# Optimization experiments

Hardware: AMD Instinct MI355X
Metric: run time of the kernel (lower is better)

The kernel has to match this reference:

```python
import jax, jax.numpy as jnp
import numpy as np

N, E, F_DIM = 30000, 480000, 256
CLS_HID, NUM_CLASS, GEN_HID, MI_HID, BATCH = 128, 16, 64, 128, 4096
COM_L1, COM_L2, LAM, ALPHA, TAU, EPS = 0.5, 0.5, 0.5, 1.0, 0.5, 1e-8


def _glorot(key, shape):
    scale = jnp.sqrt(2.0 / (shape[0] + shape[-1]))
    return scale * jax.random.normal(key, shape, dtype=jnp.float32)


def setup_inputs() -> dict:
    key = jax.random.key(0)
    ks = jax.random.split(key, 32)
    inp = {
        'feat': jax.random.normal(ks[0], (N, F_DIM), dtype=jnp.float32),
        'view1_indices': jax.random.randint(ks[1], (2, E), 0, N),
        'view1_values': jax.random.uniform(ks[2], (E,), dtype=jnp.float32),
        'view2_indices': jax.random.randint(ks[3], (2, E), 0, N),
        'view2_values': jax.random.uniform(ks[4], (E,), dtype=jnp.float32),
        'idx': jnp.sort(jax.random.randint(ks[5], (BATCH,), 0, N)),
        # GenView (v1 and v2): gen_gcn weight + gen_mlp (Linear(2*gen_hid, 1))
        'W_gen_v1': _glorot(ks[6], (F_DIM, GEN_HID)),
        'Wm_v1': _glorot(ks[7], (2 * GEN_HID, 1)),
        'bm_v1': jnp.zeros((1,), dtype=jnp.float32),
        'W_gen_v2': _glorot(ks[8], (F_DIM, GEN_HID)),
        'Wm_v2': _glorot(ks[9], (2 * GEN_HID, 1)),
        'bm_v2': jnp.zeros((1,), dtype=jnp.float32),
        # Classification: three two-layer GCN encoders (v1, v2, v)
        'W1_v1': _glorot(ks[10], (F_DIM, CLS_HID)), 'W2_v1': _glorot(ks[11], (CLS_HID, NUM_CLASS)),
        'W1_v2': _glorot(ks[12], (F_DIM, CLS_HID)), 'W2_v2': _glorot(ks[13], (CLS_HID, NUM_CLASS)),
        'W1_v': _glorot(ks[14], (F_DIM, CLS_HID)), 'W2_v': _glorot(ks[15], (CLS_HID, NUM_CLASS)),
        # MI_NCE: three single GCN layers + shared projection MLP
        'Wg': _glorot(ks[16], (F_DIM, MI_HID)),
        'Wg1': _glorot(ks[17], (F_DIM, MI_HID)),
        'Wg2': _glorot(ks[18], (F_DIM, MI_HID)),
        'Wp1': _glorot(ks[19], (MI_HID, MI_HID)), 'bp1': jnp.zeros((MI_HID,), dtype=jnp.float32),
        'Wp2': _glorot(ks[20], (MI_HID, MI_HID)), 'bp2': jnp.zeros((MI_HID,), dtype=jnp.float32),
    }
    return inp


def spmm(idx, vals, x, n):
    # sparse COO adj (idx [2,E], vals [E]) @ dense x [n,d]
    return jax.ops.segment_sum(vals[:, None] * x[idx[1]], idx[0], num_segments=n)


def gcn_layer(x, idx, vals, W, n, act):
    h = spmm(idx, vals, x @ W, n)
    return jax.nn.relu(h) if act else h


def two_layer(x, idx, vals, W1, W2, n):
    return gcn_layer(gcn_layer(x, idx, vals, W1, n, True), idx, vals, W2, n, False)


def sparse_row_softmax(scores, rows, n):
    m = jax.lax.stop_gradient(jax.ops.segment_max(scores, rows, num_segments=n))
    e = jnp.exp(scores - m[rows])
    s = jax.ops.segment_sum(e, rows, num_segments=n)
    return e / s[rows]


def gen_view(feat, idx, vals, Wg, Wm, bm, com_lambda, n):
    emb = gcn_layer(feat, idx, vals, Wg, n, True)
    ff = jnp.concatenate([emb[idx[0]], emb[idx[1]]], axis=-1)  # [E, 2*gen_hid]
    temp = (ff @ Wm + bm).reshape(-1)
    pi = sparse_row_softmax(temp, idx[0], n)  # torch.sparse.softmax(dim=1)
    return vals + com_lambda * pi  # same sparsity pattern as v_ori


def sym(idx, vals):
    # normalize1 (big=True): adj + adj.T as COO concat (duplicates sum in spmm)
    return jnp.concatenate([idx, idx[::-1]], axis=1), jnp.concatenate([vals, vals])


def get_weight(prob):
    top2 = jax.lax.top_k(prob, 2)[0]
    fir, sec = top2[:, 0], top2[:, 1]
    return jnp.exp(ALPHA * (LAM * jnp.log(fir + EPS) + (1.0 - LAM) * jnp.log(fir - sec + EPS)))


def contrast_cal(z1, z2):
    num = z1 @ z2.T
    den = jnp.linalg.norm(z1, axis=-1, keepdims=True) @ jnp.linalg.norm(z2, axis=-1, keepdims=True).T
    m12 = jnp.exp(num / den / TAU)
    m21 = m12.T
    l12 = -jnp.log(jnp.diag(m12 / (m12.sum(1, keepdims=True) + EPS)) + EPS).mean()
    l21 = -jnp.log(jnp.diag(m21 / (m21.sum(1, keepdims=True) + EPS)) + EPS).mean()
    return 0.5 * (l12 + l21)


def cogsl_forward(feat, view1_values, view2_values,
                  W_gen_v1, Wm_v1, bm_v1, W_gen_v2, Wm_v2, bm_v2,
                  W1_v1, W2_v1, W1_v2, W2_v2, W1_v, W2_v,
                  Wg, Wg1, Wg2, Wp1, bp1, Wp2, bp2,
                  view1_indices, view2_indices, idx):
    n = feat.shape[0]
    # View_Estimator (GenView + normalize1)
    nv1 = gen_view(feat, view1_indices, view1_values, W_gen_v1, Wm_v1, bm_v1, COM_L1, n)
    nv2 = gen_view(feat, view2_indices, view2_values, W_gen_v2, Wm_v2, bm_v2, COM_L2, n)
    i1, v1 = sym(view1_indices, nv1)
    i2, v2 = sym(view2_indices, nv2)
    # Classification on each generated view
    prob_v1 = jax.nn.softmax(two_layer(feat, i1, v1, W1_v1, W2_v1, n), axis=1)
    prob_v2 = jax.nn.softmax(two_layer(feat, i2, v2, W1_v2, W2_v2, n), axis=1)
    logits_v1 = jnp.log(prob_v1 + EPS)
    logits_v2 = jnp.log(prob_v2 + EPS)
    # Fusion: per-node convex combination of the two sparse views (row scaling)
    w1 = get_weight(prob_v1)
    w2 = get_weight(prob_v2)
    b1 = w1 / (w1 + w2)
    b2 = w2 / (w1 + w2)
    idx_f = jnp.concatenate([i1, i2], axis=1)
    vals_f = jnp.concatenate([b1[i1[0]] * v1, b2[i2[0]] * v2])
    prob_v = jax.nn.softmax(two_layer(feat, idx_f, vals_f, W1_v, W2_v, n), axis=1)
    logits_v = jnp.log(prob_v + EPS)
    # MI_NCE over [fused v, v1, v2], big=True -> sample `batch` nodes
    proj = lambda h: jax.nn.elu(h @ Wp1 + bp1) @ Wp2 + bp2
    ev = proj(gcn_layer(feat, idx_f, vals_f, Wg, n, True))[idx]
    e1 = proj(gcn_layer(feat, i1, v1, Wg1, n, True))[idx]
    e2 = proj(gcn_layer(feat, i2, v2, Wg2, n, True))[idx]
    vv1 = contrast_cal(ev, e1)
    vv2 = contrast_cal(ev, e2)
    v1v2 = contrast_cal(e1, e2)
    return jnp.concatenate([logits_v.ravel(), logits_v1.ravel(), logits_v2.ravel(),
                            jnp.stack([vv1, vv2, v1v2])])


def reference(feat, view1_indices, view1_values, view2_indices, view2_values, idx,
              W_gen_v1, Wm_v1, bm_v1, W_gen_v2, Wm_v2, bm_v2,
              W1_v1, W2_v1, W1_v2, W2_v2, W1_v, W2_v,
              Wg, Wg1, Wg2, Wp1, bp1, Wp2, bp2):
    return cogsl_forward(feat, view1_values, view2_values,
                         W_gen_v1, Wm_v1, bm_v1, W_gen_v2, Wm_v2, bm_v2,
                         W1_v1, W2_v1, W1_v2, W2_v2, W1_v, W2_v,
                         Wg, Wg1, Wg2, Wp1, bp1, Wp2, bp2,
                         view1_indices, view2_indices, idx)
```

## Files before the change

### kernel.cpp

```cpp
#include <hip/hip_runtime.h>
#include <math.h>

#define NN 30000
#define EE 480000
#define FD 256
#define CH 128
#define NCLS 16
#define GH 64
#define MH 128
#define BT 4096
#define EPSc 1e-8f
#define GBc ((NN + 127) / 128)
#define SPB8 ((NN + 7) / 8)
#define SPB16 ((NN + 15) / 16)
#define RBc ((BT + 15) / 16)

typedef __attribute__((ext_vector_type(8))) short short8;
typedef __attribute__((ext_vector_type(4))) float f32x4;

__device__ __forceinline__ unsigned short f2bf(float x) {
    unsigned b = __float_as_uint(x);
    unsigned r = b + 0x7FFFu + ((b >> 16) & 1u);
    return (unsigned short)(r >> 16);
}
__device__ __forceinline__ float bf2f(unsigned short h) {
    return __uint_as_float(((unsigned)h) << 16);
}
__device__ __forceinline__ float4 fma4(float s, float4 x, float4 a) {
    a.x = fmaf(s, x.x, a.x); a.y = fmaf(s, x.y, a.y);
    a.z = fmaf(s, x.z, a.z); a.w = fmaf(s, x.w, a.w);
    return a;
}

__global__ void split_bf16(const float* __restrict__ x, unsigned short* __restrict__ hi,
                           unsigned short* __restrict__ lo, long n) {
    long i = (long)blockIdx.x * 256 + threadIdx.x;
    if (i >= n) return;
    float v = x[i];
    unsigned short h = f2bf(v);
    hi[i] = h;
    lo[i] = f2bf(v - bf2f(h));
}

struct WSArgs {
    const float* s[8];
    unsigned short* h[8];
    unsigned short* l[8];
};
__global__ void wsplit_all(WSArgs a) {
    constexpr int NNp[8] = {64, 64, 128, 128, 128, 128, 128, 128};
    constexpr int OFF[9] = {0, 16384, 32768, 65536, 98304, 131072, 163840, 196608, 229376};
    int i = blockIdx.x * 256 + threadIdx.x;
    if (i >= 229376) return;
    int w = 0;
#pragma unroll
    for (int t = 1; t < 8; t++) if (i >= OFF[t]) w = t;
    int j = i - OFF[w];
    int N = NNp[w];
    int k = j / N, n = j % N;
    float v = a.s[w][j];
    unsigned short hh = f2bf(v);
    a.h[w][(size_t)n * 256 + k] = hh;
    a.l[w][(size_t)n * 256 + k] = f2bf(v - bf2f(hh));
}

template <int NT, bool OUT16>
__device__ __forceinline__ void gemm3_body(
    unsigned short* sm, int bx,
    const unsigned short* __restrict__ Ahi, const unsigned short* __restrict__ Alo,
    const unsigned short* __restrict__ BThi, const unsigned short* __restrict__ BTlo,
    int K, void* __restrict__ Cv, int Cstride, int M)
{
    unsigned short* Ah = sm;
    unsigned short* Al = Ah + 128 * 40;
    unsigned short* Bh = Al + 128 * 40;
    unsigned short* Bl = Bh + NT * 16 * 40;
    int t = threadIdx.x;
    int w = t >> 6, l = t & 63;
    int lane = l & 15, quad = l >> 4;
    int row0 = bx * 128;
    f32x4 acc[2][NT];
#pragma unroll
    for (int s = 0; s < 2; s++)
#pragma unroll
        for (int n = 0; n < NT; n++) acc[s][n] = (f32x4)(0.f);

    int ar = t >> 1, ako = (t & 1) << 4;
    int nkc = K >> 5;
    for (int kc = 0; kc < nkc; kc++) {
        int kb = kc << 5;
        {
            int gr = row0 + ar;
            float4 h0, h1, l0, l1;
            if (gr < M) {
                const float4* pH = (const float4*)&Ahi[(size_t)gr * K + kb + ako];
                const float4* pL = (const float4*)&Alo[(size_t)gr * K + kb + ako];
                h0 = pH[0]; h1 = pH[1]; l0 = pL[0]; l1 = pL[1];
            } else {
                h0 = h1 = l0 = l1 = make_float4(0.f, 0.f, 0.f, 0.f);
            }
            float4* dH = (float4*)&Ah[ar * 40 + ako];
            dH[0] = h0; dH[1] = h1;
            float4* dL = (float4*)&Al[ar * 40 + ako];
            dL[0] = l0; dL[1] = l1;
        }
        if (ar < NT * 16) {
            const float4* pH = (const float4*)&BThi[(size_t)ar * K + kb + ako];
            const float4* pL = (const float4*)&BTlo[(size_t)ar * K + kb + ako];
            float4 h0 = pH[0], h1 = pH[1], l0 = pL[0], l1 = pL[1];
            float4* dH = (float4*)&Bh[ar * 40 + ako];
            dH[0] = h0; dH[1] = h1;
            float4* dL = (float4*)&Bl[ar * 40 + ako];
            dL[0] = l0; dL[1] = l1;
        }
        __syncthreads();
        short8 aH[2], aL[2];
#pragma unroll
        for (int s = 0; s < 2; s++) {
            int r = w * 32 + s * 16 + lane;
            aH[s] = *(const short8*)&Ah[r * 40 + quad * 8];
            aL[s] = *(const short8*)&Al[r * 40 + quad * 8];
        }
#pragma unroll
        for (int n = 0; n < NT; n++) {
            int r = n * 16 + lane;
            short8 bH = *(const short8*)&Bh[r * 40 + quad * 8];
            short8 bL = *(const short8*)&Bl[r * 40 + quad * 8];
#pragma unroll
            for (int s = 0; s < 2; s++) {
                acc[s][n] = __builtin_amdgcn_mfma_f32_16x16x32_bf16(aH[s], bH, acc[s][n], 0, 0, 0);
                acc[s][n] = __builtin_amdgcn_mfma_f32_16x16x32_bf16(aH[s], bL, acc[s][n], 0, 0, 0);
                acc[s][n] = __builtin_amdgcn_mfma_f32_16x16x32_bf16(aL[s], bH, acc[s][n], 0, 0, 0);
            }
        }
        __syncthreads();
    }
#pragma unroll
    for (int s = 0; s < 2; s++) {
        int rb = row0 + w * 32 + s * 16 + quad * 4;
#pragma unroll
        for (int reg = 0; reg < 4; reg++) {
            int gr = rb + reg;
            if (gr >= M) continue;
#pragma unroll
            for (int n = 0; n < NT; n++) {
                if (OUT16)
                    ((unsigned short*)Cv)[(size_t)gr * Cstride + n * 16 + lane] = f2bf(acc[s][n][reg]);
                else
                    ((float*)Cv)[(size_t)gr * Cstride + n * 16 + lane] = acc[s][n][reg];
            }
        }
    }
}

template <int NT, bool OUT16>
__device__ __forceinline__ void gemm1_body(
    unsigned short* sm, int bx,
    const unsigned short* __restrict__ Ahi,
    const unsigned short* __restrict__ BThi,
    int K, void* __restrict__ Cv, int Cstride, int M)
{
    unsigned short* Ah = sm;
    unsigned short* Bh = Ah + 128 * 40;
    int t = threadIdx.x;
    int w = t >> 6, l = t & 63;
    int lane = l & 15, quad = l >> 4;
    int row0 = bx * 128;
    f32x4 acc[2][NT];
// ... 203 lines not shown
        v += __shfl_xor(v, 16); v += __shfl_xor(v, 32);
        if (quad == (n & 3)) atomicAdd(&scol[n * 16 + m], v);
    }
    __syncthreads();
    if (t < 128) atomicAdd(&cs[j0 + t], scol[t]);
}

__global__ __launch_bounds__(1024) void scan_block4(const int* __restrict__ cnt,
                                                    int* __restrict__ rowptr,
                                                    int* __restrict__ bsum) {
    int y = blockIdx.y;
    int* rp = rowptr + y * (NN + 1);
    int* bs = bsum + y * 32;
    __shared__ int tmp[1024];
    int t = threadIdx.x;
    int i = blockIdx.x * 1024 + t;
    int v = (i < NN) ? cnt[y * NN + i] : 0;
    tmp[t] = v;
    __syncthreads();
    for (int off = 1; off < 1024; off <<= 1) {
        int add = (t >= off) ? tmp[t - off] : 0;
        __syncthreads();
        tmp[t] += add;
        __syncthreads();
    }
    if (i <= NN) rp[i] = tmp[t] - v;
    if (t == 1023) bs[blockIdx.x] = tmp[1023];
}
__global__ void scan_bsum4(int* __restrict__ bsum, int nb) {
    bsum += blockIdx.x * 32;
    int t = threadIdx.x;
    int orig = (t < nb) ? bsum[t] : 0;
    int v = orig;
    for (int off = 1; off < 64; off <<= 1) {
        int u = __shfl_up(v, off);
        if (t >= off) v += u;
    }
    if (t < nb) bsum[t] = v - orig;
}
__global__ void scan_add4(const int* __restrict__ bsum, int* __restrict__ rowptr) {
    int y = blockIdx.y;
    const int* bs = bsum + y * 32;
    int* rp = rowptr + y * (NN + 1);
    int i = blockIdx.x * 1024 + threadIdx.x;
    if (i <= NN) rp[i] += bs[blockIdx.x];
}

__global__ __launch_bounds__(256) void gen_nv(
    const int* __restrict__ rp_d, int2* __restrict__ ed1, int2* __restrict__ ed2,
    const float* __restrict__ sb, float* __restrict__ nvd1, float* __restrict__ nvd2)
{
    int y = blockIdx.y;
    int row = blockIdx.x * 256 + threadIdx.x;
    if (row >= NN) return;
    const int* rp = rp_d + y * (NN + 1);
    int2* ed = y ? ed2 : ed1;
    float* nvd = y ? nvd2 : nvd1;
    const float* sbv = sb + (size_t)y * NN;
    int p0 = rp[row], p1 = rp[row + 1];
    float m = -3.4e38f, sum = 0.f;
    for (int j = p0; j < p1; j++) {
        float x = sbv[ed[j].x];
        if (x > m) { sum = sum * expf(m - x) + 1.f; m = x; }
        else sum += expf(x - m);
    }
    float inv = 1.f / sum;
    for (int j = p0; j < p1; j++) {
        int2 q = ed[j];
        float nv = __int_as_float(q.y) + 0.5f * expf(sbv[q.x] - m) * inv;
        nvd[j] = nv;
        ed[j].y = __float_as_int(nv);
    }
}

template <int STR4>
__device__ __forceinline__ void gath_dir_f32(
    const int* __restrict__ rp, const int2* __restrict__ ed, int row,
    const float4* __restrict__ x4, int xo, float4* a)
{
    int p0 = rp[row], p1 = rp[row + 1];
    int j = p0;
    for (; j + 8 <= p1; j += 8) {
        int2 q0 = ed[j], q1 = ed[j+1], q2 = ed[j+2], q3 = ed[j+3];
        int2 q4 = ed[j+4], q5 = ed[j+5], q6 = ed[j+6], q7 = ed[j+7];
        float4 x0 = x4[(size_t)q0.x * STR4 + xo];
        float4 x1 = x4[(size_t)q1.x * STR4 + xo];
        float4 x2 = x4[(size_t)q2.x * STR4 + xo];
        float4 x3 = x4[(size_t)q3.x * STR4 + xo];
        float4 x5 = x4[(size_t)q4.x * STR4 + xo];
        float4 x6 = x4[(size_t)q5.x * STR4 + xo];
        float4 x7 = x4[(size_t)q6.x * STR4 + xo];
        float4 x8 = x4[(size_t)q7.x * STR4 + xo];
        a[0] = fma4(__int_as_float(q0.y), x0, a[0]);
        a[1] = fma4(__int_as_float(q1.y), x1, a[1]);
        a[2] = fma4(__int_as_float(q2.y), x2, a[2]);
        a[3] = fma4(__int_as_float(q3.y), x3, a[3]);
        a[0] = fma4(__int_as_float(q4.y), x5, a[0]);
        a[1] = fma4(__int_as_float(q5.y), x6, a[1]);
        a[2] = fma4(__int_as_float(q6.y), x7, a[2]);
        a[3] = fma4(__int_as_float(q7.y), x8, a[3]);
    }
    for (; j + 4 <= p1; j += 4) {
        int2 q0 = ed[j], q1 = ed[j+1], q2 = ed[j+2], q3 = ed[j+3];
        a[0] = fma4(__int_as_float(q0.y), x4[(size_t)q0.x * STR4 + xo], a[0]);
        a[1] = fma4(__int_as_float(q1.y), x4[(size_t)q1.x * STR4 + xo], a[1]);
        a[2] = fma4(__int_as_float(q2.y), x4[(size_t)q2.x * STR4 + xo], a[2]);
        a[3] = fma4(__int_as_float(q3.y), x4[(size_t)q3.x * STR4 + xo], a[3]);
    }
    for (; j < p1; j++) {
        int2 q = ed[j];
        a[0] = fma4(__int_as_float(q.y), x4[(size_t)q.x * STR4 + xo], a[0]);
    }
}
template <int STR4>
__device__ __forceinline__ void gath_csc_f32(
    const int* __restrict__ rp, const int2* __restrict__ ec, const float* __restrict__ nvd,
    int row, const float4* __restrict__ x4, int xo, float4* a)
{
    int p0 = rp[row], p1 = rp[row + 1];
    int j = p0;
    for (; j + 8 <= p1; j += 8) {
        int2 q0 = ec[j], q1 = ec[j+1], q2 = ec[j+2], q3 = ec[j+3];
        int2 q4 = ec[j+4], q5 = ec[j+5], q6 = ec[j+6], q7 = ec[j+7];
        float4 x0 = x4[(size_t)q0.x * STR4 + xo];
        float4 x1 = x4[(size_t)q1.x * STR4 + xo];
        float4 x2 = x4[(size_t)q2.x * STR4 + xo];
        float4 x3 = x4[(size_t)q3.x * STR4 + xo];
        float4 x5 = x4[(size_t)q4.x * STR4 + xo];
        float4 x6 = x4[(size_t)q5.x * STR4 + xo];
        float4 x7 = x4[(size_t)q6.x * STR4 + xo];
        float4 x8 = x4[(size_t)q7.x * STR4 + xo];
        float v0 = nvd[q0.y], v1 = nvd[q1.y], v2 = nvd[q2.y], v3 = nvd[q3.y];
        float v4 = nvd[q4.y], v5 = nvd[q5.y], v6 = nvd[q6.y], v7 = nvd[q7.y];
        a[0] = fma4(v0, x0, a[0]);
        a[1] = fma4(v1, x1, a[1]);
        a[2] = fma4(v2, x2, a[2]);
        a[3] = fma4(v3, x3, a[3]);
        a[0] = fma4(v4, x5, a[0]);
        a[1] = fma4(v5, x6, a[1]);
        a[2] = fma4(v6, x7, a[2]);
        a[3] = fma4(v7, x8, a[3]);
    }
    for (; j + 4 <= p1; j += 4) {
        int2 q0 = ec[j], q1 = ec[j+1], q2 = ec[j+2], q3 = ec[j+3];
        float v0 = nvd[q0.y], v1 = nvd[q1.y], v2 = nvd[q2.y], v3 = nvd[q3.y];
        a[0] = fma4(v0, x4[(size_t)q0.x * STR4 + xo], a[0]);
        a[1] = fma4(v1, x4[(size_t)q1.x * STR4 + xo], a[1]);
        a[2] = fma4(v2, x4[(size_t)q2.x * STR4 + xo], a[2]);
        a[3] = fma4(v3, x4[(size_t)q3.x * STR4 + xo], a[3]);
    }
    for (; j < p1; j++) {
        int2 q = ec[j];
        a[0] = fma4(nvd[q.y], x4[(size_t)q.x * STR4 + xo], a[0]);
    }
}

__global__ __launch_bounds__(256) void spmm64_scores(
    const int* __restrict__ rp_d, const int2* __restrict__ e1, const int2* __restrict__ e2,
    const float* __restrict__ Pg, const float* __restrict__ Wm1,
    const float* __restrict__ Wm2, float* __restrict__ sb)
{
    int y = blockIdx.y;
    const int* rp = rp_d + y * (NN + 1);
    const int2* arr = y ? e2 : e1;
    int row = blockIdx.x * 16 + threadIdx.x / 16;
    int o = threadIdx.x % 16;
    if (row >= NN) return;
    float4 a[4] = {};
    gath_dir_f32<32>(rp, arr, row, (const float4*)Pg, y * 16 + o, a);
    float4 r;
    r.x = fmaxf((a[0].x + a[1].x) + (a[2].x + a[3].x), 0.f);
    r.y = fmaxf((a[0].y + a[1].y) + (a[2].y + a[3].y), 0.f);
    r.z = fmaxf((a[0].z + a[1].z) + (a[2].z + a[3].z), 0.f);
    r.w = fmaxf((a[0].w + a[1].w) + (a[2].w + a[3].w), 0.f);
    const float* Wmh = (y ? Wm2 : Wm1) + GH;
    float part = r.x * Wmh[o * 4] + r.y * Wmh[o * 4 + 1]
               + r.z * Wmh[o * 4 + 2] + r.w * Wmh[o * 4 + 3];
    part += __shfl_xor(part, 1); part += __shfl_xor(part, 2);
    part += __shfl_xor(part, 4); part += __shfl_xor(part, 8);
    if (o == 0) sb[y * NN + row] = part;
}

__device__ __forceinline__ void softmax16_epi(
    float4 r, int node, float* __restrict__ logits, float* __restrict__ wout)
{
    int o = threadIdx.x & 3;
    float mx = fmaxf(fmaxf(r.x, r.y), fmaxf(r.z, r.w));
    mx = fmaxf(mx, __shfl_xor(mx, 1));
    mx = fmaxf(mx, __shfl_xor(mx, 2));
    float e0 = expf(r.x - mx), e1 = expf(r.y - mx), e2 = expf(r.z - mx), e3 = expf(r.w - mx);
    float s = (e0 + e1) + (e2 + e3);
    s += __shfl_xor(s, 1);
    s += __shfl_xor(s, 2);
    float inv = 1.f / s;
    float p0 = e0 * inv, p1 = e1 * inv, p2 = e2 * inv, p3 = e3 * inv;
    float4 lg;
    lg.x = logf(p0 + EPSc); lg.y = logf(p1 + EPSc);
    lg.z = logf(p2 + EPSc); lg.w = logf(p3 + EPSc);
    ((float4*)logits)[(size_t)node * 4 + o] = lg;
    if (wout) {
        float f = p0, se = -1.f;
        if (p1 > f) { se = f; f = p1; } else se = p1;
        if (p2 > f) { se = f; f = p2; } else if (p2 > se) se = p2;
        if (p3 > f) { se = f; f = p3; } else if (p3 > se) se = p3;
#pragma unroll
        for (int d = 1; d <= 2; d <<= 1) {
            float of = __shfl_xor(f, d), os = __shfl_xor(se, d);
            if (of > f) { se = fmaxf(f, os); f = of; }
            else se = fmaxf(se, of);
        }
        if (o == 0)
            wout[node] = expf(0.5f * logf(f + EPSc) + 0.5f * logf(f - se + EPSc));
    }
}

__global__ __launch_bounds__(256) void spmm16_softmax_pair(
    const int* __restrict__ rp_d, const int* __restrict__ rp_c,
    const int2* __restrict__ ed1, const int2* __restrict__ ec1, const float* __restrict__ nvd1,
    const int2* __restrict__ ed2, const int2* __restrict__ ec2, const float* __restrict__ nvd2,
    const float* __restrict__ R01, float* __restrict__ logits_base, float* __restrict__ w12)
{
    int y = blockIdx.y;
    const int* rpd = rp_d + y * (NN + 1);
    const int* rpc = rp_c + y * (NN + 1);
    const int2* ed = y ? ed2 : ed1;
    const int2* ec = y ? ec2 : ec1;
    const float* nvd = y ? nvd2 : nvd1;
    int row = blockIdx.x * 64 + threadIdx.x / 4;
    int o = threadIdx.x % 4;
    if (row >= NN) return;
    const float4* x4 = (const float4*)(R01 + (size_t)y * NN * 16);
    float4 a[4] = {};
    gath_dir_f32<4>(rpd, ed, row, x4, o, a);
    gath_csc_f32<4>(rpc, ec, nvd, row, x4, o, a);
    float4 r;
    r.x = (a[0].x + a[1].x) + (a[2].x + a[3].x);
    r.y = (a[0].y + a[1].y) + (a[2].y + a[3].y);
    r.z = (a[0].z + a[1].z) + (a[2].z + a[3].z);
    r.w = (a[0].w + a[1].w) + (a[2].w + a[3].w);
    softmax16_epi(r, row, logits_base + (size_t)y * NN * NCLS, w12 + (size_t)y * NN);
}

__global__ __launch_bounds__(256) void spmm16_fused_softmax(
    const int* __restrict__ rp_d, const int* __restrict__ rp_c,
    const int2* __restrict__ ed1, const int2* __restrict__ ec1, const float* __restrict__ nvd1,
    const int2* __restrict__ ed2, const int2* __restrict__ ec2, const float* __restrict__ nvd2,
    const float* __restrict__ w12, const float* __restrict__ x, float* __restrict__ logits)
{
    int row = blockIdx.x * 64 + threadIdx.x / 4;
    int o = threadIdx.x % 4;
    if (row >= NN) return;
    const float4* x4 = (const float4*)x;
    float4 a[4] = {};
    gath_dir_f32<4>(rp_d, ed1, row, x4, o, a);
    gath_csc_f32<4>(rp_c, ec1, nvd1, row, x4, o, a);
    float4 s1;
    s1.x = (a[0].x + a[1].x) + (a[2].x + a[3].x);
    s1.y = (a[0].y + a[1].y) + (a[2].y + a[3].y);
    s1.z = (a[0].z + a[1].z) + (a[2].z + a[3].z);
    s1.w = (a[0].w + a[1].w) + (a[2].w + a[3].w);
    float4 b[4] = {};
    gath_dir_f32<4>(rp_d + (NN + 1), ed2, row, x4, o, b);
    gath_csc_f32<4>(rp_c + (NN + 1), ec2, nvd2, row, x4, o, b);
    float4 s2;
    s2.x = (b[0].x + b[1].x) + (b[2].x + b[3].x);
    s2.y = (b[0].y + b[1].y) + (b[2].y + b[3].y);
    s2.z = (b[0].z + b[1].z) + (b[2].z + b[3].z);
    s2.w = (b[0].w + b[1].w) + (b[2].w + b[3].w);
    float wa = w12[row], wb = w12[NN + row];
    float inv = 1.f / (wa + wb);
    float w1 = wa * inv, w2 = wb * inv;
    float4 r;
    r.x = w1 * s1.x + w2 * s2.x;
    r.y = w1 * s1.y + w2 * s2.y;
    r.z = w1 * s1.z + w2 * s2.z;
    r.w = w1 * s1.w + w2 * s2.w;
    softmax16_epi(r, row, logits, nullptr);
}

__device__ __forceinline__ void gath_dir_b16(
    const int* __restrict__ rp, const int2* __restrict__ ed, int row,
    const unsigned short* __restrict__ X, int xstride, int o, float* acc)
{
    int p0 = rp[row], p1 = rp[row + 1];
    int j = p0;
    for (; j + 4 <= p1; j += 4) {
        int2 q0 = ed[j], q1 = ed[j+1], q2 = ed[j+2], q3 = ed[j+3];
        short8 x0 = *(const short8*)&X[(size_t)q0.x * xstride + o * 8];
        short8 x1 = *(const short8*)&X[(size_t)q1.x * xstride + o * 8];
        short8 x2 = *(const short8*)&X[(size_t)q2.x * xstride + o * 8];
        short8 x3 = *(const short8*)&X[(size_t)q3.x * xstride + o * 8];
        float v0 = __int_as_float(q0.y), v1 = __int_as_float(q1.y);
        float v2 = __int_as_float(q2.y), v3 = __int_as_float(q3.y);
#pragma unroll
        for (int k = 0; k < 8; k++) {
            acc[k] = fmaf(v0, bf2f((unsigned short)x0[k]), acc[k]);
            acc[k] = fmaf(v1, bf2f((unsigned short)x1[k]), acc[k]);
            acc[k] = fmaf(v2, bf2f((unsigned short)x2[k]), acc[k]);
            acc[k] = fmaf(v3, bf2f((unsigned short)x3[k]), acc[k]);
        }
    }
    for (; j < p1; j++) {
        int2 q = ed[j];
        short8 xv = *(const short8*)&X[(size_t)q.x * xstride + o * 8];
        float v = __int_as_float(q.y);
#pragma unroll
        for (int k = 0; k < 8; k++)
            acc[k] = fmaf(v, bf2f((unsigned short)xv[k]), acc[k]);
    }
}
__device__ __forceinline__ void gath_csc_b16(
    const int* __restrict__ rp, const int2* __restrict__ ec, const float* __restrict__ nvd,
    int row, const unsigned short* __restrict__ X, int xstride, int o, float* acc)
{
    int p0 = rp[row], p1 = rp[row + 1];
    int j = p0;
    for (; j + 4 <= p1; j += 4) {
        int2 q0 = ec[j], q1 = ec[j+1], q2 = ec[j+2], q3 = ec[j+3];
        short8 x0 = *(const short8*)&X[(size_t)q0.x * xstride + o * 8];
        short8 x1 = *(const short8*)&X[(size_t)q1.x * xstride + o * 8];
        short8 x2 = *(const short8*)&X[(size_t)q2.x * xstride + o * 8];
        short8 x3 = *(const short8*)&X[(size_t)q3.x * xstride + o * 8];
        float v0 = nvd[q0.y], v1 = nvd[q1.y], v2 = nvd[q2.y], v3 = nvd[q3.y];
#pragma unroll
        for (int k = 0; k < 8; k++) {
            acc[k] = fmaf(v0, bf2f((unsigned short)x0[k]), acc[k]);
            acc[k] = fmaf(v1, bf2f((unsigned short)x1[k]), acc[k]);
            acc[k] = fmaf(v2, bf2f((unsigned short)x2[k]), acc[k]);
            acc[k] = fmaf(v3, bf2f((unsigned short)x3[k]), acc[k]);
        }
    }
    for (; j < p1; j++) {
        int2 q = ec[j];
        short8 xv = *(const short8*)&X[(size_t)q.x * xstride + o * 8];
        float v = nvd[q.y];
#pragma unroll
        for (int k = 0; k < 8; k++)
            acc[k] = fmaf(v, bf2f((unsigned short)xv[k]), acc[k]);
    }
}

__device__ __forceinline__ void rows_b16_body(
    int bx, int y, const int* __restrict__ rp_d, const int* __restrict__ rp_c,
    const int2* __restrict__ ed1, const int2* __restrict__ ec1, const float* __restrict__ nvd1,
    const int2* __restrict__ ed2, const int2* __restrict__ ec2, const float* __restrict__ nvd2,
    const float* __restrict__ w12, const int* __restrict__ rows,
    const unsigned short* __restrict__ Pmi, float* __restrict__ zQ)
{
    int ri = bx * 16 + threadIdx.x / 16;
    int o = threadIdx.x % 16;
    if (ri >= BT) return;
    int node = rows[ri];
    int xoff = (y == 0) ? 0 : ((y == 1) ? 128 : 256);
    const unsigned short* X = Pmi + xoff;
    float acc[8] = {};
    if (y == 0) {
        float a1[8] = {}, a2[8] = {};
        gath_dir_b16(rp_d, ed1, node, X, 384, o, a1);
        gath_csc_b16(rp_c, ec1, nvd1, node, X, 384, o, a1);
        gath_dir_b16(rp_d + (NN + 1), ed2, node, X, 384, o, a2);
        gath_csc_b16(rp_c + (NN + 1), ec2, nvd2, node, X, 384, o, a2);
        float wa = w12[node], wb = w12[NN + node];
        float inv = 1.f / (wa + wb);
        float w1 = wa * inv, w2 = wb * inv;
#pragma unroll
        for (int k = 0; k < 8; k++) acc[k] = w1 * a1[k] + w2 * a2[k];
    } else if (y == 1) {
        gath_dir_b16(rp_d, ed1, node, X, 384, o, acc);
        gath_csc_b16(rp_c, ec1, nvd1, node, X, 384, o, acc);
    } else {
        gath_dir_b16(rp_d + (NN + 1), ed2, node, X, 384, o, acc);
        gath_csc_b16(rp_c + (NN + 1), ec2, nvd2, node, X, 384, o, acc);
    }
    float* out = zQ + ((size_t)y * BT + ri) * 128 + o * 8;
#pragma unroll
    for (int k = 0; k < 8; k++) out[k] = fmaxf(acc[k], 0.f);
}

__device__ __forceinline__ void spmm128f_body(
    float* sm, int bx, int y, const int* __restrict__ rp_d, const int* __restrict__ rp_c,
    const int2* __restrict__ ed, const int2* __restrict__ ec, const float* __restrict__ nvd,
    const float* __restrict__ P01, const float* __restrict__ W2, float* __restrict__ R01)
{
    float* W2s = sm;
    float* Qs  = sm + 2048;
    for (int i = threadIdx.x; i < 2048; i += 256) W2s[i] = W2[i];
    int r = threadIdx.x / 32;
    int o = threadIdx.x % 32;
    int row = bx * 8 + r;
    float4 a[4] = {};
    if (row < NN) {
        gath_dir_f32<64>(rp_d + y * (NN + 1), ed, row, (const float4*)P01, y * 32 + o, a);
        gath_csc_f32<64>(rp_c + y * (NN + 1), ec, nvd, row, (const float4*)P01, y * 32 + o, a);
    }
    float4 q;
    q.x = fmaxf((a[0].x + a[1].x) + (a[2].x + a[3].x), 0.f);
    q.y = fmaxf((a[0].y + a[1].y) + (a[2].y + a[3].y), 0.f);
    q.z = fmaxf((a[0].z + a[1].z) + (a[2].z + a[3].z), 0.f);
    q.w = fmaxf((a[0].w + a[1].w) + (a[2].w + a[3].w), 0.f);
    *(float4*)&Qs[r * 128 + o * 4] = q;
    __syncthreads();
    int t = threadIdx.x;
    if (t < 128) {
        int rr = t >> 4, c = t & 15;
        int grow = bx * 8 + rr;
        if (grow < NN) {
            float acc = 0.f;
            const float* qrow = &Qs[rr * 128];
#pragma unroll 8
            for (int k = 0; k < 128; k++)
                acc = fmaf(qrow[k], W2s[k * 16 + c], acc);
            R01[((size_t)y * NN + grow) * 16 + c] = acc;
        }
    }
}

__device__ __forceinline__ void fused128b2_body(
    float* sm, int bx, const int* __restrict__ rp_d, const int* __restrict__ rp_c,
    const int2* __restrict__ ed1, const int2* __restrict__ ec1, const float* __restrict__ nvd1,
    const int2* __restrict__ ed2, const int2* __restrict__ ec2, const float* __restrict__ nvd2,
    const float* __restrict__ w12, const unsigned short* __restrict__ Ph2,
    const float* __restrict__ W2v, float* __restrict__ R2)
{
    float* W2s = sm;
    float* Qs  = sm + 2048;
    for (int i = threadIdx.x; i < 2048; i += 256) W2s[i] = W2v[i];
    int r = threadIdx.x / 16;
    int o = threadIdx.x % 16;
    int row = bx * 16 + r;
    float a1[8] = {}, a2[8] = {};
    float w1 = 0.f, w2 = 0.f;
    if (row < NN) {
        gath_dir_b16(rp_d, ed1, row, Ph2, 128, o, a1);
        gath_csc_b16(rp_c, ec1, nvd1, row, Ph2, 128, o, a1);
        gath_dir_b16(rp_d + (NN + 1), ed2, row, Ph2, 128, o, a2);
        gath_csc_b16(rp_c + (NN + 1), ec2, nvd2, row, Ph2, 128, o, a2);
        float wa = w12[row], wb = w12[NN + row];
        float inv = 1.f / (wa + wb);
        w1 = wa * inv; w2 = wb * inv;
    }
#pragma unroll
    for (int k = 0; k < 8; k++)
        Qs[r * 128 + o * 8 + k] = fmaxf(w1 * a1[k] + w2 * a2[k], 0.f);
    __syncthreads();
    int t = threadIdx.x;
    int rr = t >> 4, c = t & 15;
    int grow = bx * 16 + rr;
    if (grow < NN) {
        float acc = 0.f;
        const float* qrow = &Qs[rr * 128];
#pragma unroll 8
        for (int k = 0; k < 128; k++)
            acc = fmaf(qrow[k], W2s[k * 16 + c], acc);
        R2[(size_t)grow * 16 + c] = acc;
    }
}

__global__ __launch_bounds__(256) void mega2(
    const int* __restrict__ rp_d, const int* __restrict__ rp_c,
    const int2* __restrict__ ed1, const int2* __restrict__ ec1, const float* __restrict__ nvd1,
    const int2* __restrict__ ed2, const int2* __restrict__ ec2, const float* __restrict__ nvd2,
    const float* __restrict__ P01, const float* __restrict__ W2v1, const float* __restrict__ W2v2,
    float* __restrict__ R01,
    const int* __restrict__ rows, const unsigned short* __restrict__ Pmi,
    float* __restrict__ zQ)
{
    __shared__ float sm[2048 + 8 * 128];
    int b = blockIdx.x;
    if (b < 2 * SPB8) {
        int y = b / SPB8;
        spmm128f_body(sm, b % SPB8, y, rp_d, rp_c, y ? ed2 : ed1, y ? ec2 : ec1,
                      y ? nvd2 : nvd1, P01, y ? W2v2 : W2v1, R01);
        return;
    }
    b -= 2 * SPB8;
    int y = 1 + b / RBc;
    rows_b16_body(b % RBc, y, rp_d, rp_c, ed1, ec1, nvd1, ed2, ec2, nvd2,
                  nullptr, rows, Pmi, zQ);
}

__global__ __launch_bounds__(256) void mega3(
    const int* __restrict__ rp_d, const int* __restrict__ rp_c,
    const int2* __restrict__ ed1, const int2* __restrict__ ec1, const float* __restrict__ nvd1,
    const int2* __restrict__ ed2, const int2* __restrict__ ec2, const float* __restrict__ nvd2,
    const float* __restrict__ w12, const unsigned short* __restrict__ Ph2,
    const float* __restrict__ W2v, float* __restrict__ R2,
    const int* __restrict__ rows, const unsigned short* __restrict__ Pmi,
    float* __restrict__ zQ)
{
    __shared__ float sm[2048 + 16 * 128];
    int b = blockIdx.x;
    if (b < SPB16) {
        fused128b2_body(sm, b, rp_d, rp_c, ed1, ec1, nvd1, ed2, ec2, nvd2,
                        w12, Ph2, W2v, R2);
        return;
    }
    rows_b16_body(b - SPB16, 0, rp_d, rp_c, ed1, ec1, nvd1, ed2, ec2, nvd2,
                  w12, rows, Pmi, zQ);
}

__global__ __launch_bounds__(128) void proj_norm3(
    const float* __restrict__ zQ,
    const float* __restrict__ Wp1, const float* __restrict__ bp1,
    const float* __restrict__ Wp2, const float* __restrict__ bp2,
    unsigned short* __restrict__ z16)
{
    __shared__ float g[MH], u[MH];
    __shared__ float red[2];
    size_t i = (size_t)blockIdx.y * BT + blockIdx.x;
    int t = threadIdx.x;
    g[t] = zQ[i * MH + t];
    __syncthreads();
    float acc = bp1[t];
    for (int k = 0; k < MH; k++) acc = fmaf(g[k], Wp1[k * MH + t], acc);
    u[t] = acc > 0.f ? acc : (expf(acc) - 1.f);
    __syncthreads();
    float acc2 = bp2[t];
    for (int k = 0; k < MH; k++) acc2 = fmaf(u[k], Wp2[k * MH + t], acc2);
    float sq = acc2 * acc2;
#pragma unroll
    for (int off = 32; off; off >>= 1) sq += __shfl_down(sq, off);
    if ((t & 63) == 0) red[t >> 6] = sq;
    __syncthreads();
    float nrm = sqrtf(red[0] + red[1]);
    z16[i * MH + t] = f2bf(acc2 / nrm);
}

__global__ void contrast_reduce(const float* __restrict__ stats, float* __restrict__ out3)
{
    int p = blockIdx.x, t = threadIdx.x;
    const float* diag = stats + (size_t)p * 3 * BT;
    const float* rs = diag + BT;
    const float* cs = rs + BT;
    float s1 = 0.f, s2 = 0.f;
    for (int i = t; i < BT; i += 256) {
        float d = diag[i];
        s1 += logf(d / (rs[i] + EPSc) + EPSc);
        s2 += logf(d / (cs[i] + EPSc) + EPSc);
    }
#pragma unroll
    for (int off = 32; off; off >>= 1) { s1 += __shfl_down(s1, off); s2 += __shfl_down(s2, off); }
    __shared__ float sh[8];
    if ((t & 63) == 0) { sh[(t >> 6) * 2] = s1; sh[(t >> 6) * 2 + 1] = s2; }
    __syncthreads();
    if (t == 0) {
        float a = sh[0] + sh[2] + sh[4] + sh[6];
        float b = sh[1] + sh[3] + sh[5] + sh[7];
        out3[p] = 0.5f * (-a / BT - b / BT);
    }
}

extern "C" void kernel_launch(void* const* d_in, const int* in_sizes, int n_in,
                              void* d_out, int out_size, void* d_ws, size_t ws_size,
                              hipStream_t stream)
{
    const float* feat   = (const float*)d_in[0];
    const int*   ind1   = (const int*)d_in[1];
    const float* vals1  = (const float*)d_in[2];
    const int*   ind2   = (const int*)d_in[3];
    const float* vals2  = (const float*)d_in[4];
    const int*   idxb   = (const int*)d_in[5];
    const float* Wm1    = (const float*)d_in[7];
    const float* Wm2    = (const float*)d_in[10];
    const float* W2_v1  = (const float*)d_in[13];
    const float* W2_v2  = (const float*)d_in[15];
    const float* W2_v   = (const float*)d_in[17];
    const float* Wp1    = (const float*)d_in[21];
    const float* bp1    = (const float*)d_in[22];
    const float* Wp2    = (const float*)d_in[23];
    const float* bp2    = (const float*)d_in[24];
    float* dout = (float*)d_out;

    float* ws = (float*)d_ws;
    size_t off = 0;
    auto alloc = [&](size_t n) { n = (n + 3) & ~(size_t)3; float* p = ws + off; off += n; return p; };
    auto alloc_s = [&](size_t n) { return (unsigned short*)alloc((n + 1) / 2); };

    float* pool = alloc(16000000);
    float* Pg   = pool;
    float* P01  = pool + 3840000;
    float* R01  = pool + 11520000;
    float* zQ   = pool + 12480000;
    float* R2   = pool;

    unsigned short* feat_hi = alloc_s((size_t)NN * FD);
    unsigned short* feat_lo = alloc_s((size_t)NN * FD);
    unsigned short* Ph2d    = alloc_s((size_t)NN * CH);
    unsigned short* Pmi16d  = alloc_s((size_t)NN * 384);
    float* sb   = alloc(2 * NN);
    float* w12  = alloc(2 * NN);
    float* stats = alloc((size_t)3 * 3 * BT);
    unsigned short* z16 = alloc_s((size_t)3 * BT * MH);
    int2* ed1 = (int2*)alloc(2 * (size_t)EE);
    int2* ed2 = (int2*)alloc(2 * (size_t)EE);
    int2* ec1 = (int2*)alloc(2 * (size_t)EE);
    int2* ec2 = (int2*)alloc(2 * (size_t)EE);
    float* nvd1 = alloc(EE);
    float* nvd2 = alloc(EE);
    int* sd1 = (int*)alloc(EE);
    int* sd2 = (int*)alloc(EE);
    int* sc1 = (int*)alloc(EE);
    int* sc2 = (int*)alloc(EE);
    int* rp4  = (int*)alloc(4 * (NN + 1));
    int* cnt4 = (int*)alloc(4 * NN);
    int* bsum = (int*)alloc(128);
    int* rp_d = rp4;
    int* rp_c = rp4 + 2 * (NN + 1);
    unsigned short* wgen12h = alloc_s(32768); unsigned short* wgen12l = alloc_s(32768);
    unsigned short* w1pairh = alloc_s(65536); unsigned short* w1pairl = alloc_s(65536);
    unsigned short* w1vh    = alloc_s(32768); unsigned short* w1vl    = alloc_s(32768);
    unsigned short* wgallh  = alloc_s(98304); unsigned short* wgalll  = alloc_s(98304);

    const int NB = (NN + 1 + 1023) / 1024;
    const int NCNT = (EE + 255) / 256;

    hipMemsetAsync(cnt4, 0, 4 * NN * 4, stream);
    split_bf16<<<((long)NN * FD + 255) / 256, 256, 0, stream>>>(feat, feat_hi, feat_lo, (long)NN * FD);
    {
        WSArgs a;
        a.s[0] = (const float*)d_in[6];  a.h[0] = wgen12h;          a.l[0] = wgen12l;
        a.s[1] = (const float*)d_in[9];  a.h[1] = wgen12h + 16384;  a.l[1] = wgen12l + 16384;
        a.s[2] = (const float*)d_in[12]; a.h[2] = w1pairh;          a.l[2] = w1pairl;
        a.s[3] = (const float*)d_in[14]; a.h[3] = w1pairh + 32768;  a.l[3] = w1pairl + 32768;
        a.s[4] = (const float*)d_in[16]; a.h[4] = w1vh;             a.l[4] = w1vl;
        a.s[5] = (const float*)d_in[18]; a.h[5] = wgallh;           a.l[5] = wgalll;
        a.s[6] = (const float*)d_in[19]; a.h[6] = wgallh + 32768;   a.l[6] = wgalll + 32768;
        a.s[7] = (const float*)d_in[20]; a.h[7] = wgallh + 65536;   a.l[7] = wgalll + 65536;
        wsplit_all<<<(229376 + 255) / 256, 256, 0, stream>>>(a);
    }

    mega0<<<4 * GBc + NCNT, 256, 0, stream>>>(ind1, ind2, cnt4, sd1, sd2, sc1, sc2,
                                              feat_hi, w1vh, Ph2d, wgallh, Pmi16d);

    scan_block4<<<dim3(NB, 4), 1024, 0, stream>>>(cnt4, rp4, bsum);
    scan_bsum4<<<4, 64, 0, stream>>>(bsum, NB);
    scan_add4<<<dim3(NB, 4), 1024, 0, stream>>>(bsum, rp4);

    mega1<<<3 * GBc + NCNT, 256, 0, stream>>>(ind1, vals1, ind2, vals2,
                                              sd1, sd2, sc1, sc2, rp4,
                                              ed1, ec1, ed2, ec2,
                                              feat_hi, feat_lo, wgen12h, wgen12l, Pg,
                                              w1pairh, w1pairl, P01);

    spmm64_scores<<<dim3((NN + 15) / 16, 2), 256, 0, stream>>>(rp_d, ed1, ed2, Pg, Wm1, Wm2, sb);
    gen_nv<<<dim3((NN + 255) / 256, 2), 256, 0, stream>>>(rp_d, ed1, ed2, sb, nvd1, nvd2);

    mega2<<<2 * SPB8 + 2 * RBc, 256, 0, stream>>>(rp_d, rp_c, ed1, ec1, nvd1,
                                                  ed2, ec2, nvd2, P01, W2_v1, W2_v2,
                                                  R01, idxb, Pmi16d, zQ);

    spmm16_softmax_pair<<<dim3((NN + 63) / 64, 2), 256, 0, stream>>>(
        rp_d, rp_c, ed1, ec1, nvd1, ed2, ec2, nvd2, R01, dout + (size_t)NN * NCLS, w12);

    mega3<<<SPB16 + RBc, 256, 0, stream>>>(rp_d, rp_c, ed1, ec1, nvd1, ed2, ec2, nvd2,
                                           w12, Ph2d, W2_v, R2, idxb, Pmi16d, zQ);

    spmm16_fused_softmax<<<(NN + 63) / 64, 256, 0, stream>>>(
        rp_d, rp_c, ed1, ec1, nvd1, ed2, ec2, nvd2, w12, R2, dout);

    proj_norm3<<<dim3(BT, 3), 128, 0, stream>>>(zQ, Wp1, bp1, Wp2, bp2, z16);
    hipMemsetAsync(stats, 0, (size_t)3 * 3 * BT * 4, stream);
    contrast_direct<<<dim3(32, 32, 3), 256, 0, stream>>>(z16, stats);
    contrast_reduce<<<3, 256, 0, stream>>>(stats, dout + (size_t)3 * NN * NCLS);
}
```

Measured before the change: 827.8 us.

## Split 128-wide SpMM into column-sliced gathers then separate W2 projection

```diff
diff --git a/kernel.cpp b/kernel.cpp
--- a/kernel.cpp
+++ b/kernel.cpp
@@ -11,9 +11,9 @@
 #define BT 4096
 #define EPSc 1e-8f
 #define GBc ((NN + 127) / 128)
-#define SPB8 ((NN + 7) / 8)
 #define SPB16 ((NN + 15) / 16)
 #define RBc ((BT + 15) / 16)
+#define SLB ((NN + 63) / 64)
 
 typedef __attribute__((ext_vector_type(8))) short short8;
 typedef __attribute__((ext_vector_type(4))) float f32x4;
@@ -523,6 +523,86 @@
     for (; j < p1; j++) {
         int2 q = ec[j];
         a[0] = fma4(nvd[q.y], x4[(size_t)q.x * STR4 + xo], a[0]);
+    }
+}
+
+template <int STR4>
+__device__ __forceinline__ void gath_dir_f32_nt(
+    const int* __restrict__ rp, const int2* __restrict__ ed, int row,
+    const float4* __restrict__ x4, int xo, float4* a)
+{
+    int p0 = rp[row], p1 = rp[row + 1];
+    const long long* edl = (const long long*)ed;
+    int j = p0;
+    for (; j + 8 <= p1; j += 8) {
+        long long qq[8];
+#pragma unroll
+        for (int e = 0; e < 8; e++) qq[e] = __builtin_nontemporal_load(&edl[j + e]);
+        float4 x[8];
+#pragma unroll
+        for (int e = 0; e < 8; e++)
+            x[e] = x4[(size_t)(unsigned)(qq[e] & 0xffffffffLL) * STR4 + xo];
+#pragma unroll
+        for (int e = 0; e < 8; e++)
+            a[e & 3] = fma4(__int_as_float((int)(qq[e] >> 32)), x[e], a[e & 3]);
+    }
+    for (; j + 4 <= p1; j += 4) {
+        long long q0 = __builtin_nontemporal_load(&edl[j]);
+        long long q1 = __builtin_nontemporal_load(&edl[j + 1]);
+        long long q2 = __builtin_nontemporal_load(&edl[j + 2]);
+        long long q3 = __builtin_nontemporal_load(&edl[j + 3]);
+        a[0] = fma4(__int_as_float((int)(q0 >> 32)), x4[(size_t)(unsigned)(q0 & 0xffffffffLL) * STR4 + xo], a[0]);
+        a[1] = fma4(__int_as_float((int)(q1 >> 32)), x4[(size_t)(unsigned)(q1 & 0xffffffffLL) * STR4 + xo], a[1]);
+        a[2] = fma4(__int_as_float((int)(q2 >> 32)), x4[(size_t)(unsigned)(q2 & 0xffffffffLL) * STR4 + xo], a[2]);
+        a[3] = fma4(__int_as_float((int)(q3 >> 32)), x4[(size_t)(unsigned)(q3 & 0xffffffffLL) * STR4 + xo], a[3]);
+    }
+    for (; j < p1; j++) {
+        long long q = __builtin_nontemporal_load(&edl[j]);
+        a[0] = fma4(__int_as_float((int)(q >> 32)), x4[(size_t)(unsigned)(q & 0xffffffffLL) * STR4 + xo], a[0]);
+    }
+}
+template <int STR4>
+__device__ __forceinline__ void gath_csc_f32_nt(
+    const int* __restrict__ rp, const int2* __restrict__ ec, const float* __restrict__ nvd,
+    int row, const float4* __restrict__ x4, int xo, float4* a)
+{
+    int p0 = rp[row], p1 = rp[row + 1];
+    const long long* ecl = (const long long*)ec;
+    int j = p0;
+    for (; j + 8 <= p1; j += 8) {
+        long long qq[8];
+#pragma unroll
+        for (int e = 0; e < 8; e++) qq[e] = __builtin_nontemporal_load(&ecl[j + e]);
+        float4 x[8];
+#pragma unroll
+        for (int e = 0; e < 8; e++)
+            x[e] = x4[(size_t)(unsigned)(qq[e] & 0xffffffffLL) * STR4 + xo];
+        float v[8];
+#pragma unroll
+        for (int e = 0; e < 8; e++)
+            v[e] = __builtin_nontemporal_load(&nvd[(int)(qq[e] >> 32)]);
+#pragma unroll
+        for (int e = 0; e < 8; e++)
+            a[e & 3] = fma4(v[e], x[e], a[e & 3]);
+    }
+    for (; j + 4 <= p1; j += 4) {
+        long long q0 = __builtin_nontemporal_load(&ecl[j]);
+        long long q1 = __builtin_nontemporal_load(&ecl[j + 1]);
+        long long q2 = __builtin_nontemporal_load(&ecl[j + 2]);
+        long long q3 = __builtin_nontemporal_load(&ecl[j + 3]);
+        float v0 = __builtin_nontemporal_load(&nvd[(int)(q0 >> 32)]);
+        float v1 = __builtin_nontemporal_load(&nvd[(int)(q1 >> 32)]);
+        float v2 = __builtin_nontemporal_load(&nvd[(int)(q2 >> 32)]);
+        float v3 = __builtin_nontemporal_load(&nvd[(int)(q3 >> 32)]);
+        a[0] = fma4(v0, x4[(size_t)(unsigned)(q0 & 0xffffffffLL) * STR4 + xo], a[0]);
+        a[1] = fma4(v1, x4[(size_t)(unsigned)(q1 & 0xffffffffLL) * STR4 + xo], a[1]);
+        a[2] = fma4(v2, x4[(size_t)(unsigned)(q2 & 0xffffffffLL) * STR4 + xo], a[2]);
+        a[3] = fma4(v3, x4[(size_t)(unsigned)(q3 & 0xffffffffLL) * STR4 + xo], a[3]);
+    }
+    for (; j < p1; j++) {
+        long long q = __builtin_nontemporal_load(&ecl[j]);
+        float v = __builtin_nontemporal_load(&nvd[(int)(q >> 32)]);
+        a[0] = fma4(v, x4[(size_t)(unsigned)(q & 0xffffffffLL) * STR4 + xo], a[0]);
     }
 }
 
@@ -748,42 +828,63 @@
     for (int k = 0; k < 8; k++) out[k] = fmaxf(acc[k], 0.f);
 }
 
-__device__ __forceinline__ void spmm128f_body(
-    float* sm, int bx, int y, const int* __restrict__ rp_d, const int* __restrict__ rp_c,
-    const int2* __restrict__ ed, const int2* __restrict__ ec, const float* __restrict__ nvd,
-    const float* __restrict__ P01, const float* __restrict__ W2, float* __restrict__ R01)
-{
+__global__ __launch_bounds__(256) void spmm_slice(
+    const int* __restrict__ rp, const int* __restrict__ rpc,
+    const int2* __restrict__ ed, const int2* __restrict__ ec,
+    const float* __restrict__ nvd, const float* __restrict__ P01,
+    int colbase4, float* __restrict__ Qf)
+{
+    int s = blockIdx.x & 7;
+    int b = blockIdx.x >> 3;
+    int row = b * 64 + (threadIdx.x >> 2);
+    int o = threadIdx.x & 3;
+    if (row >= NN) return;
+    int xo = colbase4 + s * 4 + o;
+    float4 a[4] = {};
+    gath_dir_f32_nt<64>(rp, ed, row, (const float4*)P01, xo, a);
+    gath_csc_f32_nt<64>(rpc, ec, nvd, row, (const float4*)P01, xo, a);
+    float4 r;
+    r.x = fmaxf((a[0].x + a[1].x) + (a[2].x + a[3].x), 0.f);
+    r.y = fmaxf((a[0].y + a[1].y) + (a[2].y + a[3].y), 0.f);
+    r.z = fmaxf((a[0].z + a[1].z) + (a[2].z + a[3].z), 0.f);
+    r.w = fmaxf((a[0].w + a[1].w) + (a[2].w + a[3].w), 0.f);
+    ((float4*)Qf)[(size_t)row * 32 + s * 4 + o] = r;
+}
+
+__global__ __launch_bounds__(256) void megaC(
+    const int* __restrict__ rp_d, const int* __restrict__ rp_c,
+    const int2* __restrict__ ed1, const int2* __restrict__ ec1, const float* __restrict__ nvd1,
+    const int2* __restrict__ ed2, const int2* __restrict__ ec2, const float* __restrict__ nvd2,
+    const int* __restrict__ rows, const unsigned short* __restrict__ Pmi, float* __restrict__ zQ,
+    const float* __restrict__ Qf0, const float* __restrict__ Qf1,
+    const float* __restrict__ W2v1, const float* __restrict__ W2v2, float* __restrict__ R01)
+{
+    __shared__ float sm[4096];
+    int b = blockIdx.x;
+    if (b < 2 * RBc) {
+        int y = 1 + b / RBc;
+        rows_b16_body(b % RBc, y, rp_d, rp_c, ed1, ec1, nvd1, ed2, ec2, nvd2,
+                      nullptr, rows, Pmi, zQ);
+        return;
+    }
+    b -= 2 * RBc;
+    int y = b / SPB16, bx = b % SPB16;
+    const float* Qf = y ? Qf1 : Qf0;
+    const float* W2 = y ? W2v2 : W2v1;
     float* W2s = sm;
     float* Qs  = sm + 2048;
     for (int i = threadIdx.x; i < 2048; i += 256) W2s[i] = W2[i];
-    int r = threadIdx.x / 32;
-    int o = threadIdx.x % 32;
-    int row = bx * 8 + r;
-    float4 a[4] = {};
-    if (row < NN) {
-        gath_dir_f32<64>(rp_d + y * (NN + 1), ed, row, (const float4*)P01, y * 32 + o, a);
-        gath_csc_f32<64>(rp_c + y * (NN + 1), ec, nvd, row, (const float4*)P01, y * 32 + o, a);
-    }
-    float4 q;
-    q.x = fmaxf((a[0].x + a[1].x) + (a[2].x + a[3].x), 0.f);
-    q.y = fmaxf((a[0].y + a[1].y) + (a[2].y + a[3].y), 0.f);
-    q.z = fmaxf((a[0].z + a[1].z) + (a[2].z + a[3].z), 0.f);
-    q.w = fmaxf((a[0].w + a[1].w) + (a[2].w + a[3].w), 0.f);
-    *(float4*)&Qs[r * 128 + o * 4] = q;
+    int r = threadIdx.x >> 4, o = threadIdx.x & 15;
+    size_t row = (size_t)bx * 16 + r;
+    *(float4*)&Qs[r * 128 + o * 8]     = *(const float4*)&Qf[row * 128 + o * 8];
+    *(float4*)&Qs[r * 128 + o * 8 + 4] = *(const float4*)&Qf[row * 128 + o * 8 + 4];
     __syncthreads();
-    int t = threadIdx.x;
-    if (t < 128) {
-        int rr = t >> 4, c = t & 15;
-        int grow = bx * 8 + rr;
-        if (grow < NN) {
-            float acc = 0.f;
-            const float* qrow = &Qs[rr * 128];
+    float acc = 0.f;
+    const float* qrow = &Qs[r * 128];
 #pragma unroll 8
-            for (int k = 0; k < 128; k++)
-                acc = fmaf(qrow[k], W2s[k * 16 + c], acc);
-            R01[((size_t)y * NN + grow) * 16 + c] = acc;
-        }
-    }
+    for (int k = 0; k < 128; k++)
+        acc = fmaf(qrow[k], W2s[k * 16 + o], acc);
+    R01[((size_t)y * NN + row) * 16 + o] = acc;
 }
 
 __device__ __forceinline__ void fused128b2_body(
@@ -827,29 +928,6 @@
     }
 }
 
-__global__ __launch_bounds__(256) void mega2(
-    const int* __restrict__ rp_d, const int* __restrict__ rp_c,
-    const int2* __restrict__ ed1, const int2* __restrict__ ec1, const float* __restrict__ nvd1,
-    const int2* __restrict__ ed2, const int2* __restrict__ ec2, const float* __restrict__ nvd2,
-    const float* __restrict__ P01, const float* __restrict__ W2v1, const float* __restrict__ W2v2,
-    float* __restrict__ R01,
-    const int* __restrict__ rows, const unsigned short* __restrict__ Pmi,
-    float* __restrict__ zQ)
-{
-    __shared__ float sm[2048 + 8 * 128];
-    int b = blockIdx.x;
-    if (b < 2 * SPB8) {
-        int y = b / SPB8;
-        spmm128f_body(sm, b % SPB8, y, rp_d, rp_c, y ? ed2 : ed1, y ? ec2 : ec1,
-                      y ? nvd2 : nvd1, P01, y ? W2v2 : W2v1, R01);
-        return;
-    }
-    b -= 2 * SPB8;
-    int y = 1 + b / RBc;
-    rows_b16_body(b % RBc, y, rp_d, rp_c, ed1, ec1, nvd1, ed2, ec2, nvd2,
-                  nullptr, rows, Pmi, zQ);
-}
-
 __global__ __launch_bounds__(256) void mega3(
     const int* __restrict__ rp_d, const int* __restrict__ rp_c,
     const int2* __restrict__ ed1, const int2* __restrict__ ec1, const float* __restrict__ nvd1,
@@ -953,9 +1031,11 @@
     float* R01  = pool + 11520000;
     float* zQ   = pool + 12480000;
     float* R2   = pool;
+    float* Qf0  = pool;
 
     unsigned short* feat_hi = alloc_s((size_t)NN * FD);
     unsigned short* feat_lo = alloc_s((size_t)NN * FD);
+    float* Qf1 = (float*)feat_hi;
     unsigned short* Ph2d    = alloc_s((size_t)NN * CH);
     unsigned short* Pmi16d  = alloc_s((size_t)NN * 384);
     float* sb   = alloc(2 * NN);
@@ -1016,9 +1096,13 @@
     spmm64_scores<<<dim3((NN + 15) / 16, 2), 256, 0, stream>>>(rp_d, ed1, ed2, Pg, Wm1, Wm2, sb);
     gen_nv<<<dim3((NN + 255) / 256, 2), 256, 0, stream>>>(rp_d, ed1, ed2, sb, nvd1, nvd2);
 
-    mega2<<<2 * SPB8 + 2 * RBc, 256, 0, stream>>>(rp_d, rp_c, ed1, ec1, nvd1,
-                                                  ed2, ec2, nvd2, P01, W2_v1, W2_v2,
-                                                  R01, idxb, Pmi16d, zQ);
+    spmm_slice<<<8 * SLB, 256, 0, stream>>>(rp_d, rp_c, ed1, ec1, nvd1, P01, 0, Qf0);
+    spmm_slice<<<8 * SLB, 256, 0, stream>>>(rp_d + (NN + 1), rp_c + (NN + 1), ed2, ec2, nvd2,
+                                            P01, 32, Qf1);
+
+    megaC<<<2 * RBc + 2 * SPB16, 256, 0, stream>>>(rp_d, rp_c, ed1, ec1, nvd1,
+                                                   ed2, ec2, nvd2, idxb, Pmi16d, zQ,
+                                                   Qf0, Qf1, W2_v1, W2_v2, R01);
 
     spmm16_softmax_pair<<<dim3((NN + 63) / 64, 2), 256, 0, stream>>>(
         rp_d, rp_c, ed1, ec1, nvd1, ed2, ec2, nvd2, R01, dout + (size_t)NN * NCLS, w12);
```

Result: slower. 1.046 ms (+26.4%).
